# Performance work log

Measured on AMD Instinct MI355X. Metric: run time of the kernel, lower is better.

Reference implementation:

```python
import jax, jax.numpy as jnp
import numpy as np

B, L, D, HD = 4, 4096, 2048, 128

def setup_inputs() -> dict:
    key = jax.random.key(0)
    ks = jax.random.split(key, 9)
    s = 0.02  # keep logits in a sane range
    return {
        "x": jax.random.normal(ks[0], (B, L, D), jnp.float32),
        "Wq": jax.random.normal(ks[1], (D, HD), jnp.float32) * s,
        "bq": jax.random.normal(ks[2], (HD,), jnp.float32) * s,
        "Wk": jax.random.normal(ks[3], (D, HD), jnp.float32) * s,
        "bk": jax.random.normal(ks[4], (HD,), jnp.float32) * s,
        "Wv": jax.random.normal(ks[5], (D, HD), jnp.float32) * s,
        "bv": jax.random.normal(ks[6], (HD,), jnp.float32) * s,
        "Wo": jax.random.normal(ks[7], (HD, D), jnp.float32) * s,
        "bo": jax.random.normal(ks[8], (D,), jnp.float32) * s,
    }

def reference(x, Wq, bq, Wk, bk, Wv, bv, Wo, bo):
    # x: (B, L, D)
    q = x @ Wq + bq                      # (B, L, HD)
    k = x @ Wk + bk
    v = x @ Wv + bv
    hd = q.shape[-1]
    scores = jnp.einsum('bqd,bkd->bqk', q, k) / jnp.sqrt(jnp.float32(hd))
    Lq = x.shape[1]
    causal = jnp.tril(jnp.ones((Lq, Lq), dtype=bool))  # (L, L)
    scores = jnp.where(causal, scores, -jnp.inf)
    weights = jax.nn.softmax(scores, axis=-1)          # (B, L, L)
    out = jnp.einsum('bqk,bkd->bqd', weights, v)       # (B, L, HD)
    return out @ Wo + bo                               # (B, L, D)
```

## Files before the change

kernel.cpp:

```cpp
#include <hip/hip_runtime.h>

#define B_  4
#define L_  4096
#define D_  2048
#define HD_ 128
#define M_  (B_*L_)

typedef __attribute__((ext_vector_type(8))) short short8;
typedef __attribute__((ext_vector_type(4))) float f32x4;
typedef __attribute__((ext_vector_type(16))) float f32x16;
typedef __attribute__((ext_vector_type(4))) unsigned short u16x4;
typedef __attribute__((ext_vector_type(2))) unsigned int u32x2;
typedef __attribute__((ext_vector_type(4))) unsigned int u32x4;
typedef unsigned short u16;

#define GLL16(g, l) __builtin_amdgcn_global_load_lds( \
    (const __attribute__((address_space(1))) void*)(g), \
    (__attribute__((address_space(3))) void*)(l), 16, 0, 0)

__device__ __forceinline__ u16 f2bf(float f){
  union { float f; unsigned u; } v; v.f = f;
  unsigned r = v.u + 0x7FFFu + ((v.u >> 16) & 1u);
  return (u16)(r >> 16);
}

__device__ __forceinline__ unsigned cvtpk_bf16(float a, float b){
  unsigned r;
  asm volatile("v_cvt_pk_bf16_f32 %0, %1, %2" : "=v"(r) : "v"(a), "v"(b));
  return r;
}

__global__ __launch_bounds__(256) void prep_kernel(
    const float* __restrict__ Wq, const float* __restrict__ Wk,
    const float* __restrict__ Wv, const float* __restrict__ Wo,
    u16* __restrict__ Wf_qkv, u16* __restrict__ Wf_o)
{
  __shared__ float T[64][68];
  const int tid = threadIdx.x;
  int tb = blockIdx.x;
  int mat = tb >> 6, tt = tb & 63;
  const float* src; int Rw, Cw, rt, ct;
  if (mat < 3) {
    src = (mat==0) ? Wq : (mat==1) ? Wk : Wv;
    Rw = D_; Cw = HD_; rt = tt >> 1; ct = tt & 1;
  } else {
    src = Wo;
    Rw = HD_; Cw = D_; rt = tt >> 5; ct = tt & 31;
  }
  int r0 = rt*64, c0 = ct*64;
  #pragma unroll
  for (int i=0;i<4;i++){
    int fid = i*256 + tid;
    int row = fid >> 4, c4 = (fid & 15) * 4;
    float4 v = *reinterpret_cast<const float4*>(src + (size_t)(r0+row)*Cw + c0 + c4);
    *reinterpret_cast<float4*>(&T[row][c4]) = v;
  }
  __syncthreads();
  #pragma unroll
  for (int i=0;i<2;i++){
    int sid = i*256 + tid;
    int crow = sid >> 3, k8 = (sid & 7) * 8;
    short8 o;
    #pragma unroll
    for (int j=0;j<8;j++) o[j] = (short)f2bf(T[k8+j][crow]);
    int K = r0 + k8;
    if (mat < 3) {
      int C = mat*128 + c0 + crow;
      int t2 = K >> 6, ks = (K >> 5) & 1, lh = (K >> 3) & 3;
      int g = C >> 4, l15c = C & 15;
      size_t off = ((size_t)((t2*2 + ks)*24 + g)*64 + (lh*16 + l15c))*8;
      *reinterpret_cast<short8*>(Wf_qkv + off) = o;
    } else {
      int C = c0 + crow;
      int ks = K >> 5, lh = (K >> 3) & 3;
      int g = C >> 4, l15c = C & 15;
      size_t off = ((size_t)(ks*128 + g)*64 + (lh*16 + l15c))*8;
      *reinterpret_cast<short8*>(Wf_o + off) = o;
    }
  }
}

__global__ __launch_bounds__(256, 2) void qkv_kernel(
    const float* __restrict__ x, const u16* __restrict__ Wf,
    const float* __restrict__ bq, const float* __restrict__ bk,
    const float* __restrict__ bv,
    u16* __restrict__ Q, u16* __restrict__ Kf, u16* __restrict__ Vf)
{
  const int rb = blockIdx.x;
  const int tid  = threadIdx.x;
  const int lane = tid & 63, w = tid >> 6;
  const int l15 = lane & 15, lhi = lane >> 4;
  const int row0 = rb * 32;

  __shared__ u16 Asm[2][1024];
  __shared__ u16 Bsm[2][24*512];

  const int aR = tid >> 3, acc8 = tid & 7;
  const int ah = acc8 >> 1, ahalf = acc8 & 1;
  const int aWrOff = (aR >> 4)*512 + (ah*16 + (aR & 15))*8 + ahalf*4;
  const float* xsrc = x + (size_t)(row0 + aR)*D_ + acc8*4;

  const u16* bSrcBase = Wf + (size_t)(w*6)*512 + lane*8;
  u16* bDst0 = &Bsm[0][(w*6)*512];
  u16* bDst1 = &Bsm[1][(w*6)*512];

  f32x4 acc[2][6];
  f32x4 zero4 = {0.f,0.f,0.f,0.f};
  #pragma unroll
  for (int m=0;m<2;m++)
    #pragma unroll
    for (int n=0;n<6;n++) acc[m][n] = zero4;

  float4 xa = *reinterpret_cast<const float4*>(xsrc);
  #pragma unroll
  for (int i=0;i<6;i++)
    GLL16(bSrcBase + (size_t)i*512, bDst0 + i*512);
  {
    u16x4 a4;
    a4[0] = f2bf(xa.x); a4[1] = f2bf(xa.y); a4[2] = f2bf(xa.z); a4[3] = f2bf(xa.w);
    *reinterpret_cast<u16x4*>(&Asm[0][aWrOff]) = a4;
  }
  xa = *reinterpret_cast<const float4*>(xsrc + 32);
  __syncthreads();

  for (int t = 0; t < 64; ++t) {
    const int cur = t & 1, nxt = cur ^ 1;
    float4 xb;
    if (t + 2 < 64)
      xb = *reinterpret_cast<const float4*>(xsrc + (t+2)*32);
    if (t + 1 < 64) {
      const u16* bs = bSrcBase + (size_t)(t+1)*24*512;
      u16* bd = (nxt ? bDst1 : bDst0);
      #pragma unroll
      for (int i=0;i<6;i++)
        GLL16(bs + (size_t)i*512, bd + i*512);
    }
    short8 fa[2], fb[6];
    #pragma unroll
    for (int m=0;m<2;m++)
      fa[m] = *reinterpret_cast<const short8*>(&Asm[cur][m*512 + lane*8]);
    #pragma unroll
    for (int n=0;n<6;n++)
      fb[n] = *reinterpret_cast<const short8*>(&Bsm[cur][(w*6+n)*512 + lane*8]);
    __builtin_amdgcn_s_setprio(1);
    #pragma unroll
    for (int m=0;m<2;m++)
      #pragma unroll
      for (int n=0;n<6;n++)
        acc[m][n] = __builtin_amdgcn_mfma_f32_16x16x32_bf16(fa[m], fb[n], acc[m][n], 0, 0, 0);
    __builtin_amdgcn_s_setprio(0);
    if (t + 1 < 64) {
      u16x4 a4;
      a4[0] = f2bf(xa.x); a4[1] = f2bf(xa.y); a4[2] = f2bf(xa.z); a4[3] = f2bf(xa.w);
      *reinterpret_cast<u16x4*>(&Asm[nxt][aWrOff]) = a4;
    }
    __syncthreads();
    xa = xb;
  }

  const float qscale = 0.08838834764831845f;
  #pragma unroll
  for (int n=0;n<6;n++){
    int col = w*96 + n*16 + l15;
    int j = col >> 7;
    int c = col & 127;
    float bi = (j==0) ? bq[c] : (j==1) ? bk[c] : bv[c];
    #pragma unroll
    for (int m=0;m<2;m++){
      int rowb = row0 + m*16 + (lhi<<2);
      int bb = rowb >> 12;
      int l0 = rowb & (L_-1);
      if (j == 0) {
        #pragma unroll
        for (int r=0;r<4;r++)
          Q[(size_t)(rowb+r)*HD_ + c] = f2bf((acc[m][n][r] + bi) * qscale);
      } else if (j == 1) {
        int ksd = c >> 4, hid = (c >> 3) & 1, jd = c & 7;
        #pragma unroll
        for (int r=0;r<4;r++){
          int l = l0 + r;
          int kt = l >> 6, k6 = l & 63;
          int n2 = k6 >> 5, l31k = k6 & 31;
          Kf[((size_t)bb*64 + kt)*8192 + (n2*8 + ksd)*512 + (hid*32 + l31k)*8 + jd]
              = f2bf(acc[m][n][r] + bi);
        }
      } else {
        int nbv = (c >> 5) & 3, l31v = c & 31;
        int kt = l0 >> 6, k6 = l0 & 63;
        int ksv = k6 >> 4, hiv = (k6 >> 3) & 1, j0 = k6 & 7;
        u16x4 v4;
        #pragma unroll
        for (int r=0;r<4;r++) v4[r] = f2bf(acc[m][n][r] + bi);
        *reinterpret_cast<u16x4*>(
            Vf + ((size_t)bb*64 + kt)*8192 + (ksv*4 + nbv)*512 + (hiv*32 + l31v)*8 + j0) = v4;
      }
    }
  }
}

__global__ __launch_bounds__(256, 2) void attn_kernel(
    const u16* __restrict__ Qg, const u16* __restrict__ Kfg,
    const u16* __restrict__ Vfg, u16* __restrict__ AOf)
{
  const int blk = blockIdx.x;
  const int xcd = blk & 7;
  const int sub = blk >> 3;
  const int b   = xcd >> 1;
  const int strip = 127 - (2*sub + (xcd & 1));
  const int q0  = strip * 32;
  const int KT  = (strip >> 1) + 1;

  const int tid = threadIdx.x, lane = tid & 63, w = tid >> 6;
  const int l31 = lane & 31;
  const int hi  = lane >> 5;

  const u16* Qb  = Qg  + (size_t)b * L_ * HD_;
  const u16* Kfb = Kfg + (size_t)b * 64 * 8192 + lane*8;
  const u16* Vfb = Vfg + (size_t)b * 64 * 8192 + lane*8;

  __shared__ __attribute__((aligned(16))) float Ol[4][32][132];
  __shared__ float Ml[4][32], Ll[4][32];

  short8 qf[8];
  #pragma unroll
  for (int ks=0; ks<8; ks++)
    qf[ks] = *reinterpret_cast<const short8*>(
        &Qb[(size_t)(q0 + l31)*HD_ + ks*16 + hi*8]);

  f32x16 O[4];
  #pragma unroll
  for (int nb=0; nb<4; nb++)
    #pragma unroll
    for (int i=0;i<16;i++) O[nb][i] = 0.f;
  float m_ = -__builtin_inff();
  float l_ = 0.f;

  for (int kt = w; kt < KT; kt += 4) {
    const u16* Kt = Kfb + (size_t)kt*8192;
    f32x16 s[2];
    #pragma unroll
    for (int n=0;n<2;n++)
      #pragma unroll
      for (int i=0;i<16;i++) s[n][i] = 0.f;
    __builtin_amdgcn_s_setprio(1);
    #pragma unroll
    for (int ks=0;ks<8;ks++)
      #pragma unroll
      for (int n=0;n<2;n++){
        short8 ka = *reinterpret_cast<const short8*>(Kt + (n*8 + ks)*512);
        s[n] = __builtin_amdgcn_mfma_f32_32x32x16_bf16(ka, qf[ks], s[n], 0, 0, 0);
      }
    __builtin_amdgcn_s_setprio(0);

    if (kt == KT-1) {
      #pragma unroll
      for (int n=0;n<2;n++)
        #pragma unroll
        for (int reg=0;reg<16;reg++){
          int key = kt*64 + n*32 + (reg&3) + 8*(reg>>2) + 4*hi;
          if (key > q0 + l31) s[n][reg] = -__builtin_inff();
        }
    }

    float pmax = s[0][0];
    #pragma unroll
    for (int n=0;n<2;n++)
      #pragma unroll
      for (int reg=0;reg<16;reg++) pmax = fmaxf(pmax, s[n][reg]);
    pmax = fmaxf(pmax, __shfl_xor(pmax, 32, 64));

    if (!__all(pmax <= m_ + 8.f)) {
      float mnew = fmaxf(m_, pmax);
      float alpha = __expf(m_ - mnew);
      m_ = mnew;
      l_ *= alpha;
      #pragma unroll
      for (int nb=0; nb<4; nb++)
        #pragma unroll
        for (int i=0;i<16;i++) O[nb][i] *= alpha;
    }

    float rsum = 0.f;
    #pragma unroll
    for (int n=0;n<2;n++)
      #pragma unroll
      for (int reg=0;reg<16;reg++){
        float p = __expf(s[n][reg] - m_);
        s[n][reg] = p;
        rsum += p;
      }
    rsum += __shfl_xor(rsum, 32, 64);
    l_ += rsum;

    unsigned c[2][8], ox[2][8];
    #pragma unroll
    for (int n=0;n<2;n++)
      #pragma unroll
      for (int i=0;i<8;i++)
        c[n][i] = cvtpk_bf16(s[n][2*i], s[n][2*i+1]);
    #pragma unroll
    for (int n=0;n<2;n++)
      #pragma unroll
      for (int i=0;i<8;i++)
        ox[n][i] = (unsigned)__shfl_xor((int)c[n][i], 32, 64);

    short8 pb[4];
    #pragma unroll
    for (int n=0;n<2;n++)
      #pragma unroll
      for (int sB=0;sB<2;sB++){
        union { u32x4 u; short8 s8; } t;
        t.u[0] = hi ? ox[n][4*sB+2] : c[n][4*sB+0];
        t.u[1] = hi ? ox[n][4*sB+3] : c[n][4*sB+1];
        t.u[2] = hi ? c[n][4*sB+2]  : ox[n][4*sB+0];
        t.u[3] = hi ? c[n][4*sB+3]  : ox[n][4*sB+1];
        pb[2*n+sB] = t.s8;
      }

    const u16* Vt2 = Vfb + (size_t)kt*8192;
    __builtin_amdgcn_s_setprio(1);
    #pragma unroll
    for (int ks=0; ks<4; ks++){
      #pragma unroll
      for (int nb=0; nb<4; nb++){
        short8 av = *reinterpret_cast<const short8*>(Vt2 + (ks*4 + nb)*512);
        O[nb] = __builtin_amdgcn_mfma_f32_32x32x16_bf16(av, pb[ks], O[nb], 0, 0, 0);
      }
    }
    __builtin_amdgcn_s_setprio(0);
  }

  if (hi == 0) { Ml[w][l31] = m_; Ll[w][l31] = l_; }
  #pragma unroll
  for (int nb=0; nb<4; nb++)
    #pragma unroll
    for (int g=0; g<4; g++){
      f32x4 v;
      v[0]=O[nb][4*g+0]; v[1]=O[nb][4*g+1]; v[2]=O[nb][4*g+2]; v[3]=O[nb][4*g+3];
      *reinterpret_cast<f32x4*>(&Ol[w][l31][nb*32 + g*8 + hi*4]) = v;
    }
  __syncthreads();

  {
    int q  = tid >> 3;
    int dc = (tid & 7) * 16;
    float mw[4], lw[4];
    float M = -__builtin_inff();
    #pragma unroll
    for (int w2=0; w2<4; w2++){ mw[w2]=Ml[w2][q]; lw[w2]=Ll[w2][q]; M = fmaxf(M, mw[w2]); }
    float den = 0.f, cw[4];
    #pragma unroll
    for (int w2=0; w2<4; w2++){ float e = __expf(mw[w2]-M); cw[w2]=e; den += lw[w2]*e; }
    float inv = 1.0f/den;
    float o[16];
    #pragma unroll
    for (int j=0;j<16;j++) o[j] = 0.f;
    #pragma unroll
    for (int w2=0; w2<4; w2++){
      #pragma unroll
      for (int g=0; g<4; g++){
        f32x4 p = *reinterpret_cast<const f32x4*>(&Ol[w2][q][dc + g*4]);
        #pragma unroll
        for (int j=0;j<4;j++) o[g*4+j] += cw[w2]*p[j];
      }
    }
    short8 st0, st1;
    #pragma unroll
    for (int j=0;j<8;j++){ st0[j] = (short)f2bf(o[j]*inv); st1[j] = (short)f2bf(o[8+j]*inv); }
    size_t rowg = (size_t)b*L_ + q0 + q;
    size_t rb2g = rowg >> 5;
    int qq = (int)(rowg & 31);
    int mA = qq >> 4, l15A = qq & 15;
    int ks0 = dc >> 5,      lh0 = (dc >> 3) & 3;
    int ks1 = (dc+8) >> 5,  lh1 = ((dc+8) >> 3) & 3;
    *reinterpret_cast<short8*>(AOf + ((rb2g*4 + ks0)*2 + mA)*512 + (lh0*16 + l15A)*8) = st0;
    *reinterpret_cast<short8*>(AOf + ((rb2g*4 + ks1)*2 + mA)*512 + (lh1*16 + l15A)*8) = st1;
  }
}

__global__ __launch_bounds__(256) void proj_kernel(
    const u16* __restrict__ AOf, const u16* __restrict__ Wf_o,
    const float* __restrict__ bo, float* __restrict__ out)
{
  const int nb  = blockIdx.x;
  const int rbk = blockIdx.y;
  const int tid = threadIdx.x, lane = tid & 63, w = tid >> 6;
  const int l15 = lane & 15, lhi = lane >> 4;

  const u16* faBase = AOf  + (size_t)rbk*8*512 + lane*8;
  const u16* fbBase = Wf_o + lane*8;

  f32x4 acc[2][4];
  f32x4 zero4 = {0.f,0.f,0.f,0.f};
  #pragma unroll
  for (int m=0;m<2;m++)
    #pragma unroll
    for (int n=0;n<4;n++) acc[m][n] = zero4;

  #pragma unroll
  for (int ks=0; ks<4; ks++){
    short8 fa[2], fb[4];
    #pragma unroll
    for (int m=0;m<2;m++)
      fa[m] = *reinterpret_cast<const short8*>(faBase + (ks*2 + m)*512);
    #pragma unroll
    for (int n=0;n<4;n++)
      fb[n] = *reinterpret_cast<const short8*>(
          fbBase + (size_t)(ks*128 + nb*16 + w*4 + n)*512);
    #pragma unroll
    for (int m=0;m<2;m++)
      #pragma unroll
      for (int n=0;n<4;n++)
        acc[m][n] = __builtin_amdgcn_mfma_f32_16x16x32_bf16(fa[m], fb[n], acc[m][n], 0, 0, 0);
  }

  #pragma unroll
  for (int n=0;n<4;n++){
    int col = nb*256 + w*64 + n*16 + l15;
    float bi = bo[col];
    #pragma unroll
    for (int m=0;m<2;m++){
      int row = rbk*32 + m*16 + (lhi<<2);
      #pragma unroll
      for (int r=0;r<4;r++)
        out[(size_t)(row+r)*D_ + col] = acc[m][n][r] + bi;
    }
  }
}

extern "C" void kernel_launch(void* const* d_in, const int* in_sizes, int n_in,
                              void* d_out, int out_size, void* d_ws, size_t ws_size,
                              hipStream_t stream) {
  const float* x  = (const float*)d_in[0];
  const float* Wq = (const float*)d_in[1];
  const float* bq = (const float*)d_in[2];
  const float* Wk = (const float*)d_in[3];
  const float* bk = (const float*)d_in[4];
  const float* Wv = (const float*)d_in[5];
  const float* bv = (const float*)d_in[6];
  const float* Wo = (const float*)d_in[7];
  const float* bo = (const float*)d_in[8];
  float* out = (float*)d_out;

  u16* ws      = (u16*)d_ws;
  u16* Wf_qkv  = ws;
  u16* Wf_o    = Wf_qkv + 3*HD_*D_;
  u16* Q       = Wf_o   + (size_t)D_*HD_;
  u16* Kf      = Q + (size_t)M_*HD_;
  u16* Vf      = Kf + (size_t)M_*HD_;
  u16* AOf     = Vf + (size_t)M_*HD_;

  prep_kernel<<<256, 256, 0, stream>>>(Wq, Wk, Wv, Wo, Wf_qkv, Wf_o);
  qkv_kernel<<<512, 256, 0, stream>>>(x, Wf_qkv, bq, bk, bv, Q, Kf, Vf);
  attn_kernel<<<512, 256, 0, stream>>>(Q, Kf, Vf, AOf);
  proj_kernel<<<dim3(8, 512), 256, 0, stream>>>(AOf, Wf_o, bo, out);
}
```

Baseline: 180.7 us.

## Pre-convert x to bf16 fragment layout and stream QKV GEMM from registers

Adds a separate kernel that converts x to bf16 in an MFMA-fragment-ready layout and rewrites the QKV GEMM to load A and B fragments directly from global memory into registers. The rewritten GEMM drops LDS staging and block barriers and moves to 32x32x16 MFMAs with 64-row tiles. This removes in-loop conversion and LDS traffic, at the cost of an extra kernel that writes and rereads a 64MB bf16 copy of x. Weights are re-read per wave without LDS sharing, and the grid halves to 256 blocks.

```diff
diff --git a/kernel.cpp b/kernel.cpp
--- a/kernel.cpp
+++ b/kernel.cpp
@@ -10,13 +10,8 @@
 typedef __attribute__((ext_vector_type(4))) float f32x4;
 typedef __attribute__((ext_vector_type(16))) float f32x16;
 typedef __attribute__((ext_vector_type(4))) unsigned short u16x4;
-typedef __attribute__((ext_vector_type(2))) unsigned int u32x2;
 typedef __attribute__((ext_vector_type(4))) unsigned int u32x4;
 typedef unsigned short u16;
-
-#define GLL16(g, l) __builtin_amdgcn_global_load_lds( \
-    (const __attribute__((address_space(1))) void*)(g), \
-    (__attribute__((address_space(3))) void*)(l), 16, 0, 0)
 
 __device__ __forceinline__ u16 f2bf(float f){
   union { float f; unsigned u; } v; v.f = f;
@@ -30,7 +25,7 @@
   return r;
 }
 
-__global__ __launch_bounds__(256) void prep_kernel(
+__global__ __launch_bounds__(256) void prepw_kernel(
     const float* __restrict__ Wq, const float* __restrict__ Wk,
     const float* __restrict__ Wv, const float* __restrict__ Wo,
     u16* __restrict__ Wf_qkv, u16* __restrict__ Wf_o)
@@ -39,13 +34,13 @@
   const int tid = threadIdx.x;
   int tb = blockIdx.x;
   int mat = tb >> 6, tt = tb & 63;
-  const float* src; int Rw, Cw, rt, ct;
+  const float* src; int Cw, rt, ct;
   if (mat < 3) {
     src = (mat==0) ? Wq : (mat==1) ? Wk : Wv;
-    Rw = D_; Cw = HD_; rt = tt >> 1; ct = tt & 1;
+    Cw = HD_; rt = tt >> 1; ct = tt & 1;
   } else {
     src = Wo;
-    Rw = HD_; Cw = D_; rt = tt >> 5; ct = tt & 31;
+    Cw = D_; rt = tt >> 5; ct = tt & 31;
   }
   int r0 = rt*64, c0 = ct*64;
   #pragma unroll
@@ -66,133 +61,128 @@
     int K = r0 + k8;
     if (mat < 3) {
       int C = mat*128 + c0 + crow;
-      int t2 = K >> 6, ks = (K >> 5) & 1, lh = (K >> 3) & 3;
-      int g = C >> 4, l15c = C & 15;
-      size_t off = ((size_t)((t2*2 + ks)*24 + g)*64 + (lh*16 + l15c))*8;
+      size_t off = ((size_t)(K>>4)*12 + (C>>5))*512
+                 + ((((K>>3)&1))*32 + (C&31))*8;
       *reinterpret_cast<short8*>(Wf_qkv + off) = o;
     } else {
       int C = c0 + crow;
-      int ks = K >> 5, lh = (K >> 3) & 3;
-      int g = C >> 4, l15c = C & 15;
-      size_t off = ((size_t)(ks*128 + g)*64 + (lh*16 + l15c))*8;
+      size_t off = ((size_t)(K>>5)*128 + (C>>4))*512
+                 + ((((K>>3)&3))*16 + (C&15))*8;
       *reinterpret_cast<short8*>(Wf_o + off) = o;
     }
   }
 }
 
+__global__ __launch_bounds__(256) void prepx_kernel(
+    const float* __restrict__ x, u16* __restrict__ xbf)
+{
+  int cid  = blockIdx.x*4 + (threadIdx.x >> 6);
+  int lane = threadIdx.x & 63;
+  int l31 = lane & 31, hi = lane >> 5;
+  int rs = cid >> 7, t = cid & 127;
+  const float* src = x + (size_t)(rs*32 + l31)*D_ + t*16 + hi*8;
+  float4 f0 = *reinterpret_cast<const float4*>(src);
+  float4 f1 = *reinterpret_cast<const float4*>(src + 4);
+  union { u32x4 u; short8 s8; } o;
+  o.u[0] = cvtpk_bf16(f0.x, f0.y);
+  o.u[1] = cvtpk_bf16(f0.z, f0.w);
+  o.u[2] = cvtpk_bf16(f1.x, f1.y);
+  o.u[3] = cvtpk_bf16(f1.z, f1.w);
+  *reinterpret_cast<short8*>(xbf + (size_t)cid*512 + lane*8) = o.s8;
+}
+
 __global__ __launch_bounds__(256, 2) void qkv_kernel(
-    const float* __restrict__ x, const u16* __restrict__ Wf,
+    const u16* __restrict__ xbf, const u16* __restrict__ Wf,
     const float* __restrict__ bq, const float* __restrict__ bk,
     const float* __restrict__ bv,
     u16* __restrict__ Q, u16* __restrict__ Kf, u16* __restrict__ Vf)
 {
   const int rb = blockIdx.x;
-  const int tid  = threadIdx.x;
-  const int lane = tid & 63, w = tid >> 6;
-  const int l15 = lane & 15, lhi = lane >> 4;
-  const int row0 = rb * 32;
-
-  __shared__ u16 Asm[2][1024];
-  __shared__ u16 Bsm[2][24*512];
-
-  const int aR = tid >> 3, acc8 = tid & 7;
-  const int ah = acc8 >> 1, ahalf = acc8 & 1;
-  const int aWrOff = (aR >> 4)*512 + (ah*16 + (aR & 15))*8 + ahalf*4;
-  const float* xsrc = x + (size_t)(row0 + aR)*D_ + acc8*4;
-
-  const u16* bSrcBase = Wf + (size_t)(w*6)*512 + lane*8;
-  u16* bDst0 = &Bsm[0][(w*6)*512];
-  u16* bDst1 = &Bsm[1][(w*6)*512];
-
-  f32x4 acc[2][6];
-  f32x4 zero4 = {0.f,0.f,0.f,0.f};
+  const int tid = threadIdx.x;
+  const int lane = tid & 63, wc = tid >> 6;
+  const int l31 = lane & 31, hi = lane >> 5;
+
+  const u16* aP0 = xbf + ((size_t)(rb*2    )*128)*512 + lane*8;
+  const u16* aP1 = xbf + ((size_t)(rb*2 + 1)*128)*512 + lane*8;
+  const u16* bP  = Wf  + (size_t)(wc*3)*512 + lane*8;
+
+  f32x16 acc[2][3];
   #pragma unroll
   for (int m=0;m<2;m++)
     #pragma unroll
-    for (int n=0;n<6;n++) acc[m][n] = zero4;
-
-  float4 xa = *reinterpret_cast<const float4*>(xsrc);
-  #pragma unroll
-  for (int i=0;i<6;i++)
-    GLL16(bSrcBase + (size_t)i*512, bDst0 + i*512);
-  {
-    u16x4 a4;
-    a4[0] = f2bf(xa.x); a4[1] = f2bf(xa.y); a4[2] = f2bf(xa.z); a4[3] = f2bf(xa.w);
-    *reinterpret_cast<u16x4*>(&Asm[0][aWrOff]) = a4;
-  }
-  xa = *reinterpret_cast<const float4*>(xsrc + 32);
-  __syncthreads();
-
-  for (int t = 0; t < 64; ++t) {
-    const int cur = t & 1, nxt = cur ^ 1;
-    float4 xb;
-    if (t + 2 < 64)
-      xb = *reinterpret_cast<const float4*>(xsrc + (t+2)*32);
-    if (t + 1 < 64) {
-      const u16* bs = bSrcBase + (size_t)(t+1)*24*512;
-      u16* bd = (nxt ? bDst1 : bDst0);
-      #pragma unroll
-      for (int i=0;i<6;i++)
-        GLL16(bs + (size_t)i*512, bd + i*512);
-    }
-    short8 fa[2], fb[6];
-    #pragma unroll
-    for (int m=0;m<2;m++)
-      fa[m] = *reinterpret_cast<const short8*>(&Asm[cur][m*512 + lane*8]);
-    #pragma unroll
-    for (int n=0;n<6;n++)
-      fb[n] = *reinterpret_cast<const short8*>(&Bsm[cur][(w*6+n)*512 + lane*8]);
+    for (int nb=0;nb<3;nb++)
+      #pragma unroll
+      for (int i=0;i<16;i++) acc[m][nb][i] = 0.f;
+
+  short8 a0 = *reinterpret_cast<const short8*>(aP0);
+  short8 a1 = *reinterpret_cast<const short8*>(aP1);
+  short8 b0 = *reinterpret_cast<const short8*>(bP);
+  short8 b1 = *reinterpret_cast<const short8*>(bP + 512);
+  short8 b2 = *reinterpret_cast<const short8*>(bP + 1024);
+
+  for (int t = 0; t < 127; ++t) {
+    short8 na0 = *reinterpret_cast<const short8*>(aP0 + (size_t)(t+1)*512);
+    short8 na1 = *reinterpret_cast<const short8*>(aP1 + (size_t)(t+1)*512);
+    const u16* nb_ = bP + (size_t)(t+1)*12*512;
+    short8 nb0 = *reinterpret_cast<const short8*>(nb_);
+    short8 nb1 = *reinterpret_cast<const short8*>(nb_ + 512);
+    short8 nb2 = *reinterpret_cast<const short8*>(nb_ + 1024);
     __builtin_amdgcn_s_setprio(1);
-    #pragma unroll
-    for (int m=0;m<2;m++)
-      #pragma unroll
-      for (int n=0;n<6;n++)
-        acc[m][n] = __builtin_amdgcn_mfma_f32_16x16x32_bf16(fa[m], fb[n], acc[m][n], 0, 0, 0);
+    acc[0][0] = __builtin_amdgcn_mfma_f32_32x32x16_bf16(a0, b0, acc[0][0], 0, 0, 0);
+    acc[0][1] = __builtin_amdgcn_mfma_f32_32x32x16_bf16(a0, b1, acc[0][1], 0, 0, 0);
+    acc[0][2] = __builtin_amdgcn_mfma_f32_32x32x16_bf16(a0, b2, acc[0][2], 0, 0, 0);
+    acc[1][0] = __builtin_amdgcn_mfma_f32_32x32x16_bf16(a1, b0, acc[1][0], 0, 0, 0);
+    acc[1][1] = __builtin_amdgcn_mfma_f32_32x32x16_bf16(a1, b1, acc[1][1], 0, 0, 0);
+    acc[1][2] = __builtin_amdgcn_mfma_f32_32x32x16_bf16(a1, b2, acc[1][2], 0, 0, 0);
     __builtin_amdgcn_s_setprio(0);
-    if (t + 1 < 64) {
-      u16x4 a4;
-      a4[0] = f2bf(xa.x); a4[1] = f2bf(xa.y); a4[2] = f2bf(xa.z); a4[3] = f2bf(xa.w);
-      *reinterpret_cast<u16x4*>(&Asm[nxt][aWrOff]) = a4;
-    }
-    __syncthreads();
-    xa = xb;
-  }
+    a0 = na0; a1 = na1; b0 = nb0; b1 = nb1; b2 = nb2;
+  }
+  __builtin_amdgcn_s_setprio(1);
+  acc[0][0] = __builtin_amdgcn_mfma_f32_32x32x16_bf16(a0, b0, acc[0][0], 0, 0, 0);
+  acc[0][1] = __builtin_amdgcn_mfma_f32_32x32x16_bf16(a0, b1, acc[0][1], 0, 0, 0);
+  acc[0][2] = __builtin_amdgcn_mfma_f32_32x32x16_bf16(a0, b2, acc[0][2], 0, 0, 0);
+  acc[1][0] = __builtin_amdgcn_mfma_f32_32x32x16_bf16(a1, b0, acc[1][0], 0, 0, 0);
+  acc[1][1] = __builtin_amdgcn_mfma_f32_32x32x16_bf16(a1, b1, acc[1][1], 0, 0, 0);
+  acc[1][2] = __builtin_amdgcn_mfma_f32_32x32x16_bf16(a1, b2, acc[1][2], 0, 0, 0);
+  __builtin_amdgcn_s_setprio(0);
 
   const float qscale = 0.08838834764831845f;
-  #pragma unroll
-  for (int n=0;n<6;n++){
-    int col = w*96 + n*16 + l15;
-    int j = col >> 7;
-    int c = col & 127;
-    float bi = (j==0) ? bq[c] : (j==1) ? bk[c] : bv[c];
+  const int bb = rb >> 6, kt = rb & 63;
+  const size_t kvBase = ((size_t)bb*64 + kt)*16;
+  #pragma unroll
+  for (int nb=0; nb<3; nb++){
+    const int colbase = wc*96 + nb*32;
+    const int j = colbase >> 7;
+    const int col = colbase + l31;
+    const int c = col & 127;
+    const float bi = (j==0) ? bq[c] : (j==1) ? bk[c] : bv[c];
     #pragma unroll
     for (int m=0;m<2;m++){
-      int rowb = row0 + m*16 + (lhi<<2);
-      int bb = rowb >> 12;
-      int l0 = rowb & (L_-1);
       if (j == 0) {
         #pragma unroll
-        for (int r=0;r<4;r++)
-          Q[(size_t)(rowb+r)*HD_ + c] = f2bf((acc[m][n][r] + bi) * qscale);
+        for (int r=0;r<16;r++){
+          int row = rb*64 + m*32 + 4*hi + (r&3) + 8*(r>>2);
+          Q[(size_t)row*HD_ + c] = f2bf((acc[m][nb][r] + bi) * qscale);
+        }
       } else if (j == 1) {
         int ksd = c >> 4, hid = (c >> 3) & 1, jd = c & 7;
         #pragma unroll
-        for (int r=0;r<4;r++){
-          int l = l0 + r;
-          int kt = l >> 6, k6 = l & 63;
-          int n2 = k6 >> 5, l31k = k6 & 31;
-          Kf[((size_t)bb*64 + kt)*8192 + (n2*8 + ksd)*512 + (hid*32 + l31k)*8 + jd]
-              = f2bf(acc[m][n][r] + bi);
+        for (int r=0;r<16;r++){
+          int l31k = 8*(r>>2) + 4*hi + (r&3);
+          Kf[(kvBase + m*8 + ksd)*512 + (hid*32 + l31k)*8 + jd]
+              = f2bf(acc[m][nb][r] + bi);
         }
       } else {
-        int nbv = (c >> 5) & 3, l31v = c & 31;
-        int kt = l0 >> 6, k6 = l0 & 63;
-        int ksv = k6 >> 4, hiv = (k6 >> 3) & 1, j0 = k6 & 7;
-        u16x4 v4;
-        #pragma unroll
-        for (int r=0;r<4;r++) v4[r] = f2bf(acc[m][n][r] + bi);
-        *reinterpret_cast<u16x4*>(
-            Vf + ((size_t)bb*64 + kt)*8192 + (ksv*4 + nbv)*512 + (hiv*32 + l31v)*8 + j0) = v4;
+        int nbv = c >> 5;
+        #pragma unroll
+        for (int g=0; g<4; g++){
+          int ksv = m*2 + (g>>1), hiv = g&1, j0 = 4*hi;
+          u16x4 v4;
+          #pragma unroll
+          for (int q=0;q<4;q++) v4[q] = f2bf(acc[m][nb][4*g+q] + bi);
+          *reinterpret_cast<u16x4*>(
+              Vf + (kvBase + ksv*4 + nbv)*512 + (hiv*32 + l31)*8 + j0) = v4;
+        }
       }
     }
   }
@@ -449,9 +439,11 @@
   u16* Kf      = Q + (size_t)M_*HD_;
   u16* Vf      = Kf + (size_t)M_*HD_;
   u16* AOf     = Vf + (size_t)M_*HD_;
-
-  prep_kernel<<<256, 256, 0, stream>>>(Wq, Wk, Wv, Wo, Wf_qkv, Wf_o);
-  qkv_kernel<<<512, 256, 0, stream>>>(x, Wf_qkv, bq, bk, bv, Q, Kf, Vf);
+  u16* xbf     = AOf + (size_t)M_*HD_;
+
+  prepw_kernel<<<256, 256, 0, stream>>>(Wq, Wk, Wv, Wo, Wf_qkv, Wf_o);
+  prepx_kernel<<<16384, 256, 0, stream>>>(x, xbf);
+  qkv_kernel<<<256, 256, 0, stream>>>(xbf, Wf_qkv, bq, bk, bv, Q, Kf, Vf);
   attn_kernel<<<512, 256, 0, stream>>>(Q, Kf, Vf, AOf);
   proj_kernel<<<dim3(8, 512), 256, 0, stream>>>(AOf, Wf_o, bo, out);
 }
```

Result: slower. 195.8 us (+8.3%).
